# Performance work log

Hardware: AMD Instinct MI355X
Metric: run time of the kernel (lower is better)

Reference implementation:

```python
import jax, jax.numpy as jnp
import numpy as np

N = 50000   # nodes
E = 800000  # edges (before self-loops)
D = 96      # hidden_dim (= per-head out_channels, concat=False averages heads)
H = 4       # heads
L = 2       # num_layers
NEG_SLOPE = 0.2
EPS_BN = 1e-5


def setup_inputs() -> dict:
    key = jax.random.key(0)
    ks = jax.random.split(key, 8)
    x = jax.random.normal(ks[0], (N, D), dtype=jnp.float32)
    edge_index = jax.random.randint(ks[1], (2, E), 0, N, dtype=jnp.int64)
    # GATConv shared lin: in D -> H*D (per-head dim D), Glorot-ish scale
    W = jax.random.normal(ks[2], (L, D, H * D), dtype=jnp.float32) / np.sqrt(D).astype(np.float32)
    att_src = jax.random.normal(ks[3], (L, H, D), dtype=jnp.float32) * 0.1
    att_dst = jax.random.normal(ks[4], (L, H, D), dtype=jnp.float32) * 0.1
    bias = jnp.zeros((L, D), dtype=jnp.float32)
    gamma = jnp.ones((L, D), dtype=jnp.float32)
    beta = jnp.zeros((L, D), dtype=jnp.float32)
    return dict(x=x, edge_index=edge_index, W=W, att_src=att_src,
                att_dst=att_dst, bias=bias, gamma=gamma, beta=beta)


def _gat_layer(x, src, dst, W, a_src, a_dst, b):
    h = (x @ W).reshape(N, H, D)                      # [N,H,D]
    alpha_src = jnp.einsum('nhd,hd->nh', h, a_src)    # [N,H]
    alpha_dst = jnp.einsum('nhd,hd->nh', h, a_dst)    # [N,H]
    e = jax.nn.leaky_relu(alpha_src[src] + alpha_dst[dst], NEG_SLOPE)  # [Etot,H]
    # edge softmax grouped by destination node (numerically stable)
    m = jax.ops.segment_max(e, dst, num_segments=N)   # [N,H]
    p = jnp.exp(e - m[dst])
    denom = jax.ops.segment_sum(p, dst, num_segments=N)
    alpha = p / (denom[dst] + 1e-16)                  # [Etot,H]
    msg = h[src] * alpha[:, :, None]                  # [Etot,H,D]
    out = jax.ops.segment_sum(msg, dst, num_segments=N)  # [N,H,D]
    return out.mean(axis=1) + b                       # concat=False -> head mean


def reference(x, edge_index, W, att_src, att_dst, bias, gamma, beta):
    # PyG GATConv adds self-loops by default
    loops = jnp.arange(N, dtype=edge_index.dtype)
    ei = jnp.concatenate([edge_index, jnp.stack([loops, loops])], axis=1)
    src, dst = ei[0], ei[1]
    for l in range(L):
        x_res = x
        out = _gat_layer(x, src, dst, W[l], att_src[l], att_dst[l], bias[l])
        # BatchNorm over nodes (training-mode batch statistics, biased var)
        mu = out.mean(axis=0)
        var = out.var(axis=0)
        out = (out - mu) / jnp.sqrt(var + EPS_BN) * gamma[l] + beta[l]
        # dropout is identity at inference
        x = jax.nn.relu(out) + x_res
    return x
```

## Files before the change

kernel.cpp:

```cpp
#include <hip/hip_runtime.h>

#define DD 96
#define HH 4
#define HD 384
#define GN 32
#define NEG_SLOPE 0.2f
#define NB_STATS 128
#define SCAN_BS 1024

typedef unsigned int uint;
typedef unsigned short ushort;

__device__ inline uint pack2bf(float lo, float hi) {
    uint ulo = __float_as_uint(lo); ulo += 0x7fffu + ((ulo >> 16) & 1u);
    uint uhi = __float_as_uint(hi); uhi += 0x7fffu + ((uhi >> 16) & 1u);
    return (ulo >> 16) | (uhi & 0xffff0000u);
}

__global__ void wa_kernel(const float* __restrict__ W, const float* __restrict__ att_src,
                          const float* __restrict__ att_dst, float* __restrict__ wa) {
    const int l = blockIdx.x / DD;
    const int k = blockIdx.x % DD;
    const int t = threadIdx.x;
    const float* Wr = W + ((size_t)l * DD + k) * HD;
    const float* as = att_src + (size_t)l * HD;
    const float* ad = att_dst + (size_t)l * HD;
    const bool hiHalf = t >= 32;
    float s0=0,s1=0,s2=0,s3=0,d0=0,d1=0,d2=0,d3=0;
    int c; float w, ps, pd;
    c = t;       w = Wr[c]; s0 = fmaf(w, as[c], s0); d0 = fmaf(w, ad[c], d0);
    c = t + 64;  w = Wr[c]; ps = w * as[c]; pd = w * ad[c];
    s0 += hiHalf ? 0.f : ps;  s1 += hiHalf ? ps : 0.f;
    d0 += hiHalf ? 0.f : pd;  d1 += hiHalf ? pd : 0.f;
    c = t + 128; w = Wr[c]; s1 = fmaf(w, as[c], s1); d1 = fmaf(w, ad[c], d1);
    c = t + 192; w = Wr[c]; s2 = fmaf(w, as[c], s2); d2 = fmaf(w, ad[c], d2);
    c = t + 256; w = Wr[c]; ps = w * as[c]; pd = w * ad[c];
    s2 += hiHalf ? 0.f : ps;  s3 += hiHalf ? ps : 0.f;
    d2 += hiHalf ? 0.f : pd;  d3 += hiHalf ? pd : 0.f;
    c = t + 320; w = Wr[c]; s3 = fmaf(w, as[c], s3); d3 = fmaf(w, ad[c], d3);
#pragma unroll
    for (int off = 32; off; off >>= 1) {
        s0 += __shfl_xor(s0, off); s1 += __shfl_xor(s1, off);
        s2 += __shfl_xor(s2, off); s3 += __shfl_xor(s3, off);
        d0 += __shfl_xor(d0, off); d1 += __shfl_xor(d1, off);
        d2 += __shfl_xor(d2, off); d3 += __shfl_xor(d3, off);
    }
    if (t == 0) {
        float* o = wa + ((size_t)l * DD + k) * 8;
        o[0]=s0; o[1]=d0; o[2]=s1; o[3]=d1; o[4]=s2; o[5]=d2; o[6]=s3; o[7]=d3;
    }
}

__global__ void __launch_bounds__(256) gemm_kernel(const float* __restrict__ x,
        const float* __restrict__ W, const float* __restrict__ wa,
        uint* __restrict__ hp, float* __restrict__ asrc, float* __restrict__ adst, int N) {
    __shared__ float xs[GN * 100];
    __shared__ float was[DD * 8];
    const int t = threadIdx.x;
    const int n0 = blockIdx.x * GN;
    const int nvalid = min(GN, N - n0);

    for (int i = t; i < DD * 8; i += 256) was[i] = wa[i];
    {
        const float4* xsrc = (const float4*)(x + (size_t)n0 * DD);
        const int lim = (nvalid * DD) / 4;
        for (int i4 = t; i4 < lim; i4 += 256) {
            const float4 v = xsrc[i4];
            const int node = i4 / 24, k = (i4 % 24) * 4;
            float* dp = &xs[node * 100 + k];
            dp[0] = v.x; dp[1] = v.y; dp[2] = v.z; dp[3] = v.w;
        }
    }
    __syncthreads();

    const int lane = t & 63;
    const int nb = (t >> 6) * 8;
    float acc[8][6];
#pragma unroll
    for (int nn = 0; nn < 8; nn++)
#pragma unroll
        for (int j = 0; j < 6; j++) acc[nn][j] = 0.f;

    for (int k = 0; k < DD; k++) {
        float wv[6];
#pragma unroll
        for (int j = 0; j < 6; j++) wv[j] = W[(size_t)k * HD + j * 64 + lane];
#pragma unroll
        for (int nn = 0; nn < 8; nn++) {
            const float xv = xs[(nb + nn) * 100 + k];
#pragma unroll
            for (int j = 0; j < 6; j++) acc[nn][j] = fmaf(xv, wv[j], acc[nn][j]);
        }
    }
#pragma unroll
    for (int nn = 0; nn < 8; nn++) {
        if (nb + nn < nvalid) {
            uint* hr = hp + (size_t)(n0 + nb + nn) * 192;
            hr[lane]       = pack2bf(acc[nn][0], acc[nn][1]);
            hr[64 + lane]  = pack2bf(acc[nn][2], acc[nn][3]);
            hr[128 + lane] = pack2bf(acc[nn][4], acc[nn][5]);
        }
    }
    {
        const int nn = t >> 3, j = t & 7;
        if (nn < nvalid) {
            const float* xr = &xs[nn * 100];
            float s = 0.f;
            for (int k = 0; k < DD; k++) s = fmaf(xr[k], was[k * 8 + j], s);
            const int n = n0 + nn, h = j >> 1;
            if ((j & 1) == 0) asrc[n * 4 + h] = s;
            else              adst[n * 4 + h] = s;
        }
    }
}

__global__ void count_kernel(const int* __restrict__ ei, int* __restrict__ deg, int E) {
    int i = blockIdx.x * blockDim.x + threadIdx.x;
    const int stride = gridDim.x * blockDim.x;
    for (; i < E; i += stride) atomicAdd(&deg[ei[E + i]], 1);
}

__global__ void scan1_kernel(const int* __restrict__ deg, int* __restrict__ locpre,
                             int* __restrict__ bsum, int N) {
    __shared__ int ts[256];
    const int t = threadIdx.x;
    const int base = blockIdx.x * SCAN_BS + t * 4;
    int e0 = 0, e1 = 0, e2 = 0, e3 = 0;
    if (base + 3 < N) {
        const int4 v = *(const int4*)(deg + base);
        e0 = v.x + 1; e1 = v.y + 1; e2 = v.z + 1; e3 = v.w + 1;
    } else {
        if (base     < N) e0 = deg[base]     + 1;
        if (base + 1 < N) e1 = deg[base + 1] + 1;
        if (base + 2 < N) e2 = deg[base + 2] + 1;
        if (base + 3 < N) e3 = deg[base + 3] + 1;
    }
    const int s = e0 + e1 + e2 + e3;
    ts[t] = s;
    __syncthreads();
    for (int off = 1; off < 256; off <<= 1) {
        const int u = (t >= off) ? ts[t - off] : 0;
        __syncthreads();
        ts[t] += u;
        __syncthreads();
    }
    const int ex = ts[t] - s;
    if (base + 3 < N) {
        *(int4*)(locpre + base) = make_int4(ex, ex + e0, ex + e0 + e1, ex + e0 + e1 + e2);
    } else if (base < N) {
        locpre[base] = ex;
        if (base + 1 < N) locpre[base + 1] = ex + e0;
        if (base + 2 < N) locpre[base + 2] = ex + e0 + e1;
    }
    if (t == 255) bsum[blockIdx.x] = ts[255];
}

__global__ void scan2_kernel(int* __restrict__ bsum, int* __restrict__ rowptr,
                             int NBLK, int N) {
    const int t = threadIdx.x;
    const int mine = (t < NBLK) ? bsum[t] : 0;
    int v = mine;
#pragma unroll
    for (int off = 1; off < 64; off <<= 1) {
        const int u = __shfl_up(v, off);
        if (t >= off) v += u;
    }
    if (t < NBLK) bsum[t] = v - mine;
    if (t == 63) rowptr[N] = v;
}

__global__ void scan3_kernel(const int* __restrict__ locpre, const int* __restrict__ bsum,
                             int* __restrict__ rowptr, int* __restrict__ cursor, int N) {
    const int base = blockIdx.x * SCAN_BS + threadIdx.x * 4;
    const int boff = bsum[blockIdx.x];
    if (base + 3 < N) {
        int4 v = *(const int4*)(locpre + base);
        v.x += boff; v.y += boff; v.z += boff; v.w += boff;
        *(int4*)(rowptr + base) = v;
        *(int4*)(cursor + base) = v;
    } else {
        for (int i = base; i < N; i++) {
            const int r = locpre[i] + boff;
            rowptr[i] = r; cursor[i] = r;
        }
    }
}

__global__ void scatter_kernel(const int* __restrict__ ei, int* __restrict__ cursor,
                               const int* __restrict__ rowptr, int* __restrict__ col,
                               int E, int Etot) {
    int i = blockIdx.x * blockDim.x + threadIdx.x;
    const int stride = gridDim.x * blockDim.x;
    for (; i < Etot; i += stride) {
        if (i < E) {
            const int src = ei[i], dst = ei[E + i];
            col[atomicAdd(&cursor[dst], 1)] = src;
        } else {
            const int n = i - E;
            col[rowptr[n + 1] - 1] = n;
        }
    }
}

#define EDGE_W(av, w0, w1, w2, w3, cf1, cf4)                                          \
    { float t0 = av.x + adv.x, t1 = av.y + adv.y, t2 = av.z + adv.z, t3 = av.w + adv.w; \
      t0 = t0 > 0.f ? t0 : NEG_SLOPE * t0;  t1 = t1 > 0.f ? t1 : NEG_SLOPE * t1;      \
      t2 = t2 > 0.f ? t2 : NEG_SLOPE * t2;  t3 = t3 > 0.f ? t3 : NEG_SLOPE * t3;      \
      w0 = __expf(t0); w1 = __expf(t1); w2 = __expf(t2); w3 = __expf(t3);             \
      den0 += w0; den1 += w1; den2 += w2; den3 += w3;                                 \
      cf1 = hi32 ? w1 : w0; cf4 = hi32 ? w3 : w2; }

#define EDGE_FMA(u0, u1, u2, w0, w1, w2, w3, cf1, cf4)                                \
    { acc0 = fmaf(__uint_as_float(u0 << 16), w0, acc0);                               \
      acc1 = fmaf(__uint_as_float(u0 & 0xffff0000u), cf1, acc1);                      \
      acc2 = fmaf(__uint_as_float(u1 << 16), w1, acc2);                               \
      acc3 = fmaf(__uint_as_float(u1 & 0xffff0000u), w2, acc3);                       \
      acc4 = fmaf(__uint_as_float(u2 << 16), cf4, acc4);                              \
      acc5 = fmaf(__uint_as_float(u2 & 0xffff0000u), w3, acc5); }

__global__ void agg_csr_kernel(const int* __restrict__ rowptr, const int* __restrict__ col,
                               const uint* __restrict__ hp, const float* __restrict__ asrc,
                               const float* __restrict__ adst, const float* __restrict__ bias,
                               float* __restrict__ y, int N) {
    const int lane = threadIdx.x & 63;
    const bool hi32 = lane >= 32;
    const int n = (blockIdx.x * blockDim.x + threadIdx.x) >> 6;
    if (n >= N) return;
    const int beg = rowptr[n], endp = rowptr[n + 1];
    const float4 adv = *(const float4*)(adst + (size_t)n * 4);
    float acc0=0,acc1=0,acc2=0,acc3=0,acc4=0,acc5=0;
    float den0=0,den1=0,den2=0,den3=0;
    int e = beg;
    for (; e + 4 <= endp; e += 4) {
        const int s0 = col[e], s1 = col[e + 1], s2 = col[e + 2], s3 = col[e + 3];
        const float4 av0 = *(const float4*)(asrc + (size_t)s0 * 4);
        const float4 av1 = *(const float4*)(asrc + (size_t)s1 * 4);
        const float4 av2 = *(const float4*)(asrc + (size_t)s2 * 4);
        const float4 av3 = *(const float4*)(asrc + (size_t)s3 * 4);
        const uint* h0 = hp + (size_t)s0 * 192 + lane;
        const uint* h1 = hp + (size_t)s1 * 192 + lane;
        const uint* h2 = hp + (size_t)s2 * 192 + lane;
        const uint* h3 = hp + (size_t)s3 * 192 + lane;
        const uint u00 = h0[0], u01 = h0[64], u02 = h0[128];
        const uint u10 = h1[0], u11 = h1[64], u12 = h1[128];
        const uint u20 = h2[0], u21 = h2[64], u22 = h2[128];
        const uint u30 = h3[0], u31 = h3[64], u32 = h3[128];
        float w0,w1,w2,w3,cf1,cf4;
        EDGE_W(av0, w0, w1, w2, w3, cf1, cf4);
        EDGE_FMA(u00, u01, u02, w0, w1, w2, w3, cf1, cf4);
        EDGE_W(av1, w0, w1, w2, w3, cf1, cf4);
        EDGE_FMA(u10, u11, u12, w0, w1, w2, w3, cf1, cf4);
        EDGE_W(av2, w0, w1, w2, w3, cf1, cf4);
        EDGE_FMA(u20, u21, u22, w0, w1, w2, w3, cf1, cf4);
        EDGE_W(av3, w0, w1, w2, w3, cf1, cf4);
        EDGE_FMA(u30, u31, u32, w0, w1, w2, w3, cf1, cf4);
    }
    for (; e < endp; e++) {
        const int s0 = col[e];
        const float4 av0 = *(const float4*)(asrc + (size_t)s0 * 4);
        const uint* h0 = hp + (size_t)s0 * 192 + lane;
        const uint u00 = h0[0], u01 = h0[64], u02 = h0[128];
        float w0,w1,w2,w3,cf1,cf4;
        EDGE_W(av0, w0, w1, w2, w3, cf1, cf4);
        EDGE_FMA(u00, u01, u02, w0, w1, w2, w3, cf1, cf4);
    }
    const float r0 = 1.f / (den0 + 1e-16f);
    const float r1 = 1.f / (den1 + 1e-16f);
    const float r2 = 1.f / (den2 + 1e-16f);
    const float r3 = 1.f / (den3 + 1e-16f);
    const float rc1 = hi32 ? r1 : r0;
    const float rc4 = hi32 ? r3 : r2;
    const float A = acc0 * r0  + acc3 * r2;
    const float B = acc1 * rc1 + acc4 * rc4;
    const float C = acc2 * r1  + acc5 * r3;
    const float shB = __shfl_xor(B, 32);
    const float shC = __shfl_xor(C, 32);
    float* yr = y + (size_t)n * DD;
    yr[lane] = 0.25f * (A + (hi32 ? shC : shB)) + bias[lane];
    if (!hi32) yr[64 + lane] = 0.25f * (B + shC) + bias[64 + lane];
}

__global__ void bnstats_kernel(const float* __restrict__ y, float* __restrict__ pbuf,
                               int total4) {
    __shared__ float ps[384 * 4];
    __shared__ float qs[384 * 4];
    const int t = threadIdx.x;
    const int stride = gridDim.x * 384;
    float s0=0,s1=0,s2=0,s3=0,q0=0,q1=0,q2=0,q3=0;
    for (int i = blockIdx.x * 384 + t; i < total4; i += stride) {
        const float4 v = ((const float4*)y)[i];
        s0 += v.x; q0 = fmaf(v.x, v.x, q0);
        s1 += v.y; q1 = fmaf(v.y, v.y, q1);
        s2 += v.z; q2 = fmaf(v.z, v.z, q2);
        s3 += v.w; q3 = fmaf(v.w, v.w, q3);
    }
    ps[t*4+0]=s0; ps[t*4+1]=s1; ps[t*4+2]=s2; ps[t*4+3]=s3;
    qs[t*4+0]=q0; qs[t*4+1]=q1; qs[t*4+2]=q2; qs[t*4+3]=q3;
    __syncthreads();
    if (t < 192) {
        const int d = t % 96;
        const float* src = (t < 96) ? ps : qs;
        float r = 0.f;
#pragma unroll
        for (int m = 0; m < 16; m++) r += src[d + 96 * m];
        pbuf[blockIdx.x * 192 + t] = r;
    }
}

__global__ void bnfin_kernel(const float* __restrict__ pbuf, const float* __restrict__ gamma,
                             const float* __restrict__ beta, float* __restrict__ scsh, int N) {
    const int d = threadIdx.x;
    float s = 0.f, q = 0.f;
    for (int b = 0; b < NB_STATS; b++) {
        s += pbuf[b * 192 + d];
        q += pbuf[b * 192 + 96 + d];
    }
    const float invN = 1.f / (float)N;
    const float mu = s * invN;
    const float var = q * invN - mu * mu;
    const float sc = gamma[d] * rsqrtf(var + 1e-5f);
    scsh[d] = sc;
    scsh[d + DD] = beta[d] - mu * sc;
}

__global__ void bn_apply_kernel(const float* __restrict__ y, const float* __restrict__ scsh,
                                const float* __restrict__ xin, float* __restrict__ xout,
                                int total4) {
    int i = blockIdx.x * blockDim.x + threadIdx.x;
    const int stride = gridDim.x * blockDim.x;
    for (; i < total4; i += stride) {
        const int d4 = (i % 24) * 4;
        const float4 v = ((const float4*)y)[i];
        const float4 xi = ((const float4*)xin)[i];
        float4 o; float a;
        a = fmaf(v.x, scsh[d4],     scsh[d4 + DD]);     o.x = (a > 0.f ? a : 0.f) + xi.x;
        a = fmaf(v.y, scsh[d4 + 1], scsh[d4 + 1 + DD]); o.y = (a > 0.f ? a : 0.f) + xi.y;
        a = fmaf(v.z, scsh[d4 + 2], scsh[d4 + 2 + DD]); o.z = (a > 0.f ? a : 0.f) + xi.z;
        a = fmaf(v.w, scsh[d4 + 3], scsh[d4 + 3 + DD]); o.w = (a > 0.f ? a : 0.f) + xi.w;
        ((float4*)xout)[i] = o;
    }
}

extern "C" void kernel_launch(void* const* d_in, const int* in_sizes, int n_in,
                              void* d_out, int out_size, void* d_ws, size_t ws_size,
                              hipStream_t stream) {
    const float* x        = (const float*)d_in[0];
    const int*   ei       = (const int*)d_in[1];
    const float* W        = (const float*)d_in[2];
    const float* att_src  = (const float*)d_in[3];
    const float* att_dst  = (const float*)d_in[4];
    const float* bias     = (const float*)d_in[5];
    const float* gamma    = (const float*)d_in[6];
    const float* beta     = (const float*)d_in[7];
    float* out_final = (float*)d_out;

    const int N = in_sizes[0] / DD;
    const int E = in_sizes[1] / 2;
    const int Etot = E + N;
    const int NBLK = (N + SCAN_BS - 1) / SCAN_BS;

    char* ws = (char*)d_ws;
    size_t off = 0;
    auto alloc = [&](size_t bytes) -> void* {
        void* p = ws + off;
        off += (bytes + 255) & ~(size_t)255;
        return p;
    };
    uint*  hp     = (uint*)alloc((size_t)N * 192 * 4);
    float* asrc   = (float*)alloc((size_t)N * HH * 4);
    float* adst   = (float*)alloc((size_t)N * HH * 4);
    float* y      = (float*)alloc((size_t)N * DD * 4);
    float* xbuf   = (float*)alloc((size_t)N * DD * 4);
    float* pbuf   = (float*)alloc((size_t)NB_STATS * 192 * 4);
    float* scsh   = (float*)alloc(2 * DD * 4);
    float* wa     = (float*)alloc(2 * DD * 8 * 4);
    int*   deg    = (int*)alloc((size_t)N * 4);
    int*   locpre = (int*)alloc((size_t)N * 4);
    int*   bsum   = (int*)alloc(64 * 4);
    int*   rowptr = (int*)alloc((size_t)(N + 1) * 4);
    int*   cursor = (int*)alloc((size_t)N * 4);
    int*   colidx = (int*)alloc((size_t)Etot * 4);

    hipMemsetAsync(deg, 0, (size_t)N * 4, stream);
    count_kernel<<<1024, 256, 0, stream>>>(ei, deg, E);
    scan1_kernel<<<NBLK, 256, 0, stream>>>(deg, locpre, bsum, N);
    scan2_kernel<<<1, 64, 0, stream>>>(bsum, rowptr, NBLK, N);
    scan3_kernel<<<NBLK, 256, 0, stream>>>(locpre, bsum, rowptr, cursor, N);
    scatter_kernel<<<1024, 256, 0, stream>>>(ei, cursor, rowptr, colidx, E, Etot);
    wa_kernel<<<2 * DD, 64, 0, stream>>>(W, att_src, att_dst, wa);

    for (int l = 0; l < 2; l++) {
        const float* xin = (l == 0) ? x : xbuf;
        float* xout = (l == 1) ? out_final : xbuf;

        gemm_kernel<<<(N + GN - 1) / GN, 256, 0, stream>>>(
            xin, W + (size_t)l * DD * HD, wa + (size_t)l * DD * 8, hp, asrc, adst, N);
        agg_csr_kernel<<<(N * 64 + 255) / 256, 256, 0, stream>>>(
            rowptr, colidx, hp, asrc, adst, bias + (size_t)l * DD, y, N);
        bnstats_kernel<<<NB_STATS, 384, 0, stream>>>(y, pbuf, N * DD / 4);
        bnfin_kernel<<<1, DD, 0, stream>>>(pbuf, gamma + (size_t)l * DD,
                                           beta + (size_t)l * DD, scsh, N);
        bn_apply_kernel<<<2048, 256, 0, stream>>>(y, scsh, xin, xout, N * DD / 4);
    }
}
```

Measured before the change: 469.9 us.

## Precompute edge attention weights and softmax denominators in separate kernels

Moves the per-edge leaky-relu and exp out of the aggregation kernel. A new edge-parallel kernel writes one float4 of weights per edge, and a per-node kernel sums them into reciprocal denominators with the head mean folded in. The aggregation kernel then only loads precomputed weights instead of computing exp redundantly in all 64 lanes of a wavefront. This removes redundant transcendental work but adds two kernel launches per layer, a dst array, and extra global traffic of about 13 MB per layer for the edge weights. The max-subtraction is still omitted, as before.

New measurement: 485.6 us. 1.03x slower.

```diff
diff --git a/kernel.cpp b/kernel.cpp
--- a/kernel.cpp
+++ b/kernel.cpp
@@ -188,55 +188,81 @@
 
 __global__ void scatter_kernel(const int* __restrict__ ei, int* __restrict__ cursor,
                                const int* __restrict__ rowptr, int* __restrict__ col,
-                               int E, int Etot) {
+                               int* __restrict__ dstarr, int E, int Etot) {
     int i = blockIdx.x * blockDim.x + threadIdx.x;
     const int stride = gridDim.x * blockDim.x;
     for (; i < Etot; i += stride) {
         if (i < E) {
             const int src = ei[i], dst = ei[E + i];
-            col[atomicAdd(&cursor[dst], 1)] = src;
+            const int pos = atomicAdd(&cursor[dst], 1);
+            col[pos] = src;
+            dstarr[pos] = dst;
         } else {
             const int n = i - E;
-            col[rowptr[n + 1] - 1] = n;
-        }
-    }
-}
-
-#define EDGE_W(av, w0, w1, w2, w3, cf1, cf4)                                          \
-    { float t0 = av.x + adv.x, t1 = av.y + adv.y, t2 = av.z + adv.z, t3 = av.w + adv.w; \
-      t0 = t0 > 0.f ? t0 : NEG_SLOPE * t0;  t1 = t1 > 0.f ? t1 : NEG_SLOPE * t1;      \
-      t2 = t2 > 0.f ? t2 : NEG_SLOPE * t2;  t3 = t3 > 0.f ? t3 : NEG_SLOPE * t3;      \
-      w0 = __expf(t0); w1 = __expf(t1); w2 = __expf(t2); w3 = __expf(t3);             \
-      den0 += w0; den1 += w1; den2 += w2; den3 += w3;                                 \
-      cf1 = hi32 ? w1 : w0; cf4 = hi32 ? w3 : w2; }
-
-#define EDGE_FMA(u0, u1, u2, w0, w1, w2, w3, cf1, cf4)                                \
-    { acc0 = fmaf(__uint_as_float(u0 << 16), w0, acc0);                               \
+            const int pos = rowptr[n + 1] - 1;
+            col[pos] = n;
+            dstarr[pos] = n;
+        }
+    }
+}
+
+__global__ void ew_kernel(const int* __restrict__ col, const int* __restrict__ dstarr,
+                          const float* __restrict__ asrc, const float* __restrict__ adst,
+                          float4* __restrict__ ew4, int Etot) {
+    int i = blockIdx.x * blockDim.x + threadIdx.x;
+    const int stride = gridDim.x * blockDim.x;
+    for (; i < Etot; i += stride) {
+        const int s = col[i], d = dstarr[i];
+        const float4 av = ((const float4*)asrc)[s];
+        const float4 dv = ((const float4*)adst)[d];
+        float e0 = av.x + dv.x, e1 = av.y + dv.y, e2 = av.z + dv.z, e3 = av.w + dv.w;
+        e0 = e0 > 0.f ? e0 : NEG_SLOPE * e0;
+        e1 = e1 > 0.f ? e1 : NEG_SLOPE * e1;
+        e2 = e2 > 0.f ? e2 : NEG_SLOPE * e2;
+        e3 = e3 > 0.f ? e3 : NEG_SLOPE * e3;
+        ew4[i] = make_float4(__expf(e0), __expf(e1), __expf(e2), __expf(e3));
+    }
+}
+
+__global__ void den_kernel(const int* __restrict__ rowptr, const float4* __restrict__ ew4,
+                           float4* __restrict__ rden, int N) {
+    const int n = blockIdx.x * blockDim.x + threadIdx.x;
+    if (n >= N) return;
+    const int beg = rowptr[n], endp = rowptr[n + 1];
+    float s0 = 0.f, s1 = 0.f, s2 = 0.f, s3 = 0.f;
+    for (int i = beg; i < endp; i++) {
+        const float4 w = ew4[i];
+        s0 += w.x; s1 += w.y; s2 += w.z; s3 += w.w;
+    }
+    rden[n] = make_float4(0.25f / (s0 + 1e-16f), 0.25f / (s1 + 1e-16f),
+                          0.25f / (s2 + 1e-16f), 0.25f / (s3 + 1e-16f));
+}
+
+#define EDGE_FMA(u0, u1, u2, w4)                                                      \
+    { const float cf1 = hi32 ? w4.y : w4.x;                                           \
+      const float cf4 = hi32 ? w4.w : w4.z;                                           \
+      acc0 = fmaf(__uint_as_float(u0 << 16), w4.x, acc0);                             \
       acc1 = fmaf(__uint_as_float(u0 & 0xffff0000u), cf1, acc1);                      \
-      acc2 = fmaf(__uint_as_float(u1 << 16), w1, acc2);                               \
-      acc3 = fmaf(__uint_as_float(u1 & 0xffff0000u), w2, acc3);                       \
+      acc2 = fmaf(__uint_as_float(u1 << 16), w4.y, acc2);                             \
+      acc3 = fmaf(__uint_as_float(u1 & 0xffff0000u), w4.z, acc3);                     \
       acc4 = fmaf(__uint_as_float(u2 << 16), cf4, acc4);                              \
-      acc5 = fmaf(__uint_as_float(u2 & 0xffff0000u), w3, acc5); }
+      acc5 = fmaf(__uint_as_float(u2 & 0xffff0000u), w4.w, acc5); }
 
 __global__ void agg_csr_kernel(const int* __restrict__ rowptr, const int* __restrict__ col,
-                               const uint* __restrict__ hp, const float* __restrict__ asrc,
-                               const float* __restrict__ adst, const float* __restrict__ bias,
+                               const uint* __restrict__ hp, const float4* __restrict__ ew4,
+                               const float4* __restrict__ rden, const float* __restrict__ bias,
                                float* __restrict__ y, int N) {
     const int lane = threadIdx.x & 63;
     const bool hi32 = lane >= 32;
     const int n = (blockIdx.x * blockDim.x + threadIdx.x) >> 6;
     if (n >= N) return;
     const int beg = rowptr[n], endp = rowptr[n + 1];
-    const float4 adv = *(const float4*)(adst + (size_t)n * 4);
     float acc0=0,acc1=0,acc2=0,acc3=0,acc4=0,acc5=0;
-    float den0=0,den1=0,den2=0,den3=0;
     int e = beg;
     for (; e + 4 <= endp; e += 4) {
         const int s0 = col[e], s1 = col[e + 1], s2 = col[e + 2], s3 = col[e + 3];
-        const float4 av0 = *(const float4*)(asrc + (size_t)s0 * 4);
-        const float4 av1 = *(const float4*)(asrc + (size_t)s1 * 4);
-        const float4 av2 = *(const float4*)(asrc + (size_t)s2 * 4);
-        const float4 av3 = *(const float4*)(asrc + (size_t)s3 * 4);
+        const float4 wA = ew4[e],     wB = ew4[e + 1];
+        const float4 wC = ew4[e + 2], wD = ew4[e + 3];
         const uint* h0 = hp + (size_t)s0 * 192 + lane;
         const uint* h1 = hp + (size_t)s1 * 192 + lane;
         const uint* h2 = hp + (size_t)s2 * 192 + lane;
@@ -245,39 +271,29 @@
         const uint u10 = h1[0], u11 = h1[64], u12 = h1[128];
         const uint u20 = h2[0], u21 = h2[64], u22 = h2[128];
         const uint u30 = h3[0], u31 = h3[64], u32 = h3[128];
-        float w0,w1,w2,w3,cf1,cf4;
-        EDGE_W(av0, w0, w1, w2, w3, cf1, cf4);
-        EDGE_FMA(u00, u01, u02, w0, w1, w2, w3, cf1, cf4);
-        EDGE_W(av1, w0, w1, w2, w3, cf1, cf4);
-        EDGE_FMA(u10, u11, u12, w0, w1, w2, w3, cf1, cf4);
-        EDGE_W(av2, w0, w1, w2, w3, cf1, cf4);
-        EDGE_FMA(u20, u21, u22, w0, w1, w2, w3, cf1, cf4);
-        EDGE_W(av3, w0, w1, w2, w3, cf1, cf4);
-        EDGE_FMA(u30, u31, u32, w0, w1, w2, w3, cf1, cf4);
+        EDGE_FMA(u00, u01, u02, wA);
+        EDGE_FMA(u10, u11, u12, wB);
+        EDGE_FMA(u20, u21, u22, wC);
+        EDGE_FMA(u30, u31, u32, wD);
     }
     for (; e < endp; e++) {
         const int s0 = col[e];
-        const float4 av0 = *(const float4*)(asrc + (size_t)s0 * 4);
+        const float4 wA = ew4[e];
         const uint* h0 = hp + (size_t)s0 * 192 + lane;
         const uint u00 = h0[0], u01 = h0[64], u02 = h0[128];
-        float w0,w1,w2,w3,cf1,cf4;
-        EDGE_W(av0, w0, w1, w2, w3, cf1, cf4);
-        EDGE_FMA(u00, u01, u02, w0, w1, w2, w3, cf1, cf4);
-    }
-    const float r0 = 1.f / (den0 + 1e-16f);
-    const float r1 = 1.f / (den1 + 1e-16f);
-    const float r2 = 1.f / (den2 + 1e-16f);
-    const float r3 = 1.f / (den3 + 1e-16f);
-    const float rc1 = hi32 ? r1 : r0;
-    const float rc4 = hi32 ? r3 : r2;
-    const float A = acc0 * r0  + acc3 * r2;
-    const float B = acc1 * rc1 + acc4 * rc4;
-    const float C = acc2 * r1  + acc5 * r3;
+        EDGE_FMA(u00, u01, u02, wA);
+    }
+    const float4 rd = rden[n];
+    const float rc1 = hi32 ? rd.y : rd.x;
+    const float rc4 = hi32 ? rd.w : rd.z;
+    const float A = acc0 * rd.x + acc3 * rd.z;
+    const float B = acc1 * rc1  + acc4 * rc4;
+    const float C = acc2 * rd.y + acc5 * rd.w;
     const float shB = __shfl_xor(B, 32);
     const float shC = __shfl_xor(C, 32);
     float* yr = y + (size_t)n * DD;
-    yr[lane] = 0.25f * (A + (hi32 ? shC : shB)) + bias[lane];
-    if (!hi32) yr[64 + lane] = 0.25f * (B + shC) + bias[64 + lane];
+    yr[lane] = A + (hi32 ? shC : shB) + bias[lane];
+    if (!hi32) yr[64 + lane] = B + shC + bias[64 + lane];
 }
 
 __global__ void bnstats_kernel(const float* __restrict__ y, float* __restrict__ pbuf,
@@ -366,27 +382,30 @@
         off += (bytes + 255) & ~(size_t)255;
         return p;
     };
-    uint*  hp     = (uint*)alloc((size_t)N * 192 * 4);
-    float* asrc   = (float*)alloc((size_t)N * HH * 4);
-    float* adst   = (float*)alloc((size_t)N * HH * 4);
-    float* y      = (float*)alloc((size_t)N * DD * 4);
-    float* xbuf   = (float*)alloc((size_t)N * DD * 4);
-    float* pbuf   = (float*)alloc((size_t)NB_STATS * 192 * 4);
-    float* scsh   = (float*)alloc(2 * DD * 4);
-    float* wa     = (float*)alloc(2 * DD * 8 * 4);
-    int*   deg    = (int*)alloc((size_t)N * 4);
-    int*   locpre = (int*)alloc((size_t)N * 4);
-    int*   bsum   = (int*)alloc(64 * 4);
-    int*   rowptr = (int*)alloc((size_t)(N + 1) * 4);
-    int*   cursor = (int*)alloc((size_t)N * 4);
-    int*   colidx = (int*)alloc((size_t)Etot * 4);
+    uint*   hp     = (uint*)alloc((size_t)N * 192 * 4);
+    float*  asrc   = (float*)alloc((size_t)N * HH * 4);
+    float*  adst   = (float*)alloc((size_t)N * HH * 4);
+    float*  y      = (float*)alloc((size_t)N * DD * 4);
+    float*  xbuf   = (float*)alloc((size_t)N * DD * 4);
+    float*  pbuf   = (float*)alloc((size_t)NB_STATS * 192 * 4);
+    float*  scsh   = (float*)alloc(2 * DD * 4);
+    float*  wa     = (float*)alloc(2 * DD * 8 * 4);
+    int*    deg    = (int*)alloc((size_t)N * 4);
+    int*    locpre = (int*)alloc((size_t)N * 4);
+    int*    bsum   = (int*)alloc(64 * 4);
+    int*    rowptr = (int*)alloc((size_t)(N + 1) * 4);
+    int*    cursor = (int*)alloc((size_t)N * 4);
+    int*    colidx = (int*)alloc((size_t)Etot * 4);
+    int*    dstarr = (int*)alloc((size_t)Etot * 4);
+    float4* ew4    = (float4*)alloc((size_t)Etot * 16);
+    float4* rden   = (float4*)alloc((size_t)N * 16);
 
     hipMemsetAsync(deg, 0, (size_t)N * 4, stream);
     count_kernel<<<1024, 256, 0, stream>>>(ei, deg, E);
     scan1_kernel<<<NBLK, 256, 0, stream>>>(deg, locpre, bsum, N);
     scan2_kernel<<<1, 64, 0, stream>>>(bsum, rowptr, NBLK, N);
     scan3_kernel<<<NBLK, 256, 0, stream>>>(locpre, bsum, rowptr, cursor, N);
-    scatter_kernel<<<1024, 256, 0, stream>>>(ei, cursor, rowptr, colidx, E, Etot);
+    scatter_kernel<<<1024, 256, 0, stream>>>(ei, cursor, rowptr, colidx, dstarr, E, Etot);
     wa_kernel<<<2 * DD, 64, 0, stream>>>(W, att_src, att_dst, wa);
 
     for (int l = 0; l < 2; l++) {
@@ -395,8 +414,10 @@
 
         gemm_kernel<<<(N + GN - 1) / GN, 256, 0, stream>>>(
             xin, W + (size_t)l * DD * HD, wa + (size_t)l * DD * 8, hp, asrc, adst, N);
+        ew_kernel<<<2048, 256, 0, stream>>>(colidx, dstarr, asrc, adst, ew4, Etot);
+        den_kernel<<<(N + 255) / 256, 256, 0, stream>>>(rowptr, ew4, rden, N);
         agg_csr_kernel<<<(N * 64 + 255) / 256, 256, 0, stream>>>(
-            rowptr, colidx, hp, asrc, adst, bias + (size_t)l * DD, y, N);
+            rowptr, colidx, hp, ew4, rden, bias + (size_t)l * DD, y, N);
         bnstats_kernel<<<NB_STATS, 384, 0, stream>>>(y, pbuf, N * DD / 4);
         bnfin_kernel<<<1, DD, 0, stream>>>(pbuf, gamma + (size_t)l * DD,
                                            beta + (size_t)l * DD, scsh, N);
```
